# Kernel tuning notes

Measured on AMD Instinct MI355X. Metric: run time of the kernel, lower is better.

The kernel has to match this reference:

```python
import jax, jax.numpy as jnp
import numpy as np

B, L, D = 4, 2048, 512
H = 8
DH = D // H  # 64
SCALE = DH // H  # faithful to source: key.size(-1)//num_heads = 64//8 = 8 (multiplicative)
LN_EPS = 1e-5


def setup_inputs() -> dict:
    key = jax.random.key(0)
    ks = jax.random.split(key, 16)
    s = 1.0 / np.sqrt(D)
    inp = {
        "query": jax.random.normal(ks[0], (B, L, D), jnp.float32),
        "key": jax.random.normal(ks[1], (B, L, D), jnp.float32),
        "value": jax.random.normal(ks[2], (B, L, D), jnp.float32),
        "Wq": jax.random.uniform(ks[3], (D, D), jnp.float32, -s, s),
        "bq": jax.random.uniform(ks[4], (D,), jnp.float32, -s, s),
        "Wk": jax.random.uniform(ks[5], (D, D), jnp.float32, -s, s),
        "bk": jax.random.uniform(ks[6], (D,), jnp.float32, -s, s),
        "Wv": jax.random.uniform(ks[7], (D, D), jnp.float32, -s, s),
        "bv": jax.random.uniform(ks[8], (D,), jnp.float32, -s, s),
        "Wo": jax.random.uniform(ks[9], (D, D), jnp.float32, -s, s),
        "bo": jax.random.uniform(ks[10], (D,), jnp.float32, -s, s),
        "gamma": jnp.ones((D,), jnp.float32),
        "beta": jnp.zeros((D,), jnp.float32),
    }
    return inp


def _layer_norm(x, gamma, beta):
    mu = jnp.mean(x, axis=-1, keepdims=True)
    var = jnp.mean(jnp.square(x - mu), axis=-1, keepdims=True)
    return (x - mu) * jax.lax.rsqrt(var + LN_EPS) * gamma + beta


def reference(query, key, value, Wq, bq, Wk, bk, Wv, bv, Wo, bo, gamma, beta):
    res = query
    # QKV projections: [B, L, D]
    q = query @ Wq.T + bq
    k = key @ Wk.T + bk
    v = value @ Wv.T + bv
    # faithful to source: raw view(B*H, -1, DH) with NO transpose
    q = q.reshape(B * H, -1, DH)
    k = k.reshape(B * H, -1, DH)
    v = v.reshape(B * H, -1, DH)
    # bmm -> multiplicative scale -> softmax(dim=2) -> bmm
    attn = jnp.einsum('bqd,bkd->bqk', q, k) * SCALE  # [B*H, L, L]
    attn = jax.nn.softmax(attn, axis=2)
    ctx = jnp.einsum('bqk,bkd->bqd', attn, v)        # [B*H, L, DH]
    ctx = ctx.reshape(B, -1, DH * H)                  # [B, L, D]
    out = ctx @ Wo.T + bo
    out = _layer_norm(res + out, gamma, beta)
    return (out, attn)
```

## Files before the change

kernel.cpp:

```cpp
#include <hip/hip_runtime.h>

#define LSEQ 2048
#define DMODEL 512
#define DHD 64
#define SLAB (LSEQ*DHD)

typedef __attribute__((ext_vector_type(8))) short short8;
typedef __attribute__((ext_vector_type(4))) float f32x4;
typedef float f4raw __attribute__((ext_vector_type(4)));
typedef _Float16 half8 __attribute__((ext_vector_type(8)));
typedef _Float16 h4_t  __attribute__((ext_vector_type(4)));

__device__ __forceinline__ short f2bf(float x) {
    union { float f; unsigned u; } v; v.f = x;
    unsigned r = v.u + 0x7FFF + ((v.u >> 16) & 1);
    return (short)(r >> 16);
}
__device__ __forceinline__ float bf2f(short h) {
    union { float f; unsigned u; } v; v.u = ((unsigned)(unsigned short)h) << 16;
    return v.f;
}

#define GLOAD_LDS16(g, l) __builtin_amdgcn_global_load_lds( \
    (const __attribute__((address_space(1))) void*)(g),     \
    (__attribute__((address_space(3))) void*)(l), 16, 0, 0)

#define VMCNT0()  asm volatile("s_waitcnt vmcnt(0)" ::: "memory")
#define VMCNT2()  asm volatile("s_waitcnt vmcnt(2)" ::: "memory")
#define VMCNT4()  asm volatile("s_waitcnt vmcnt(4)" ::: "memory")
#define VMCNT6()  asm volatile("s_waitcnt vmcnt(6)" ::: "memory")
#define LGKM0()   asm volatile("s_waitcnt lgkmcnt(0)" ::: "memory")
#define BARRIER() do { __builtin_amdgcn_s_barrier(); __builtin_amdgcn_sched_barrier(0); } while (0)

template<int MODE>
__global__ __launch_bounds__(256) void proj_gemm(
    const float* __restrict__ A, const float* __restrict__ W,
    const float* __restrict__ bias, float* __restrict__ Cf,
    short* __restrict__ C0)
{
    __shared__ __align__(16) short Ah[64][40], Al[64][40], Bh[64][40], Bl[64][40];

    const int tid  = threadIdx.x;
    const int lane = tid & 63, wv = tid >> 6;
    const int wm = wv >> 1, wn = wv & 1;
    const int fr = lane & 15, kg = lane >> 4;
    const int m0 = blockIdx.y * 64, n0 = blockIdx.x * 64;

    f32x4 acc[2][2];
    #pragma unroll
    for (int i = 0; i < 2; ++i)
        #pragma unroll
        for (int j = 0; j < 2; ++j) { f32x4 z = {0.f,0.f,0.f,0.f}; acc[i][j] = z; }

    const int srow = tid >> 2, sc8 = (tid & 3) << 3;

    for (int kt = 0; kt < 16; ++kt) {
        __syncthreads();
        {
            const float* ap = A + (size_t)(m0 + srow) * DMODEL + kt*32 + sc8;
            float4 a0 = *(const float4*)ap;
            float4 a1 = *(const float4*)(ap + 4);
            float va[8] = {a0.x,a0.y,a0.z,a0.w,a1.x,a1.y,a1.z,a1.w};
            short8 h, l;
            #pragma unroll
            for (int j = 0; j < 8; ++j) { short hh = f2bf(va[j]); h[j] = hh; l[j] = f2bf(va[j] - bf2f(hh)); }
            *(short8*)&Ah[srow][sc8] = h; *(short8*)&Al[srow][sc8] = l;

            const float* wp = W + (size_t)(n0 + srow) * DMODEL + kt*32 + sc8;
            float4 b0 = *(const float4*)wp;
            float4 b1 = *(const float4*)(wp + 4);
            float vb[8] = {b0.x,b0.y,b0.z,b0.w,b1.x,b1.y,b1.z,b1.w};
            #pragma unroll
            for (int j = 0; j < 8; ++j) { short hh = f2bf(vb[j]); h[j] = hh; l[j] = f2bf(vb[j] - bf2f(hh)); }
            *(short8*)&Bh[srow][sc8] = h; *(short8*)&Bl[srow][sc8] = l;
        }
        __syncthreads();

        short8 ah[2], al[2], bh[2], bl[2];
        #pragma unroll
        for (int mf = 0; mf < 2; ++mf) {
            ah[mf] = *(short8*)&Ah[wm*32 + mf*16 + fr][kg*8];
            al[mf] = *(short8*)&Al[wm*32 + mf*16 + fr][kg*8];
        }
        #pragma unroll
        for (int nf = 0; nf < 2; ++nf) {
            bh[nf] = *(short8*)&Bh[wn*32 + nf*16 + fr][kg*8];
            bl[nf] = *(short8*)&Bl[wn*32 + nf*16 + fr][kg*8];
        }
        #pragma unroll
        for (int mf = 0; mf < 2; ++mf)
            #pragma unroll
            for (int nf = 0; nf < 2; ++nf) {
                acc[mf][nf] = __builtin_amdgcn_mfma_f32_16x16x32_bf16(ah[mf], bh[nf], acc[mf][nf], 0,0,0);
                acc[mf][nf] = __builtin_amdgcn_mfma_f32_16x16x32_bf16(ah[mf], bl[nf], acc[mf][nf], 0,0,0);
                acc[mf][nf] = __builtin_amdgcn_mfma_f32_16x16x32_bf16(al[mf], bh[nf], acc[mf][nf], 0,0,0);
            }
    }

    #pragma unroll
    for (int mf = 0; mf < 2; ++mf)
        #pragma unroll
        for (int nf = 0; nf < 2; ++nf) {
            const int col = n0 + wn*32 + nf*16 + fr;
            const float bv = bias[col];
            #pragma unroll
            for (int r = 0; r < 4; ++r) {
                const int row = m0 + wm*32 + mf*16 + kg*4 + r;
                const float o = acc[mf][nf][r] + bv;
                const size_t idx = (size_t)row * DMODEL + col;
                if (MODE == 0) Cf[idx] = o;
                else           ((_Float16*)C0)[idx] = (_Float16)o;
            }
        }
}

__global__ __launch_bounds__(256) void vtransf_kernel(
    const short* __restrict__ vh, short* __restrict__ vtf)
{
    __shared__ short T[64][72];
    const int tid = threadIdx.x;
    const int s  = blockIdx.y;
    const int t0 = blockIdx.x * 64;
    const size_t slab = (size_t)s * SLAB;

    {
        const int r = tid >> 2, c0 = (tid & 3) << 4;
        const short* src = vh + slab + (size_t)(t0 + r) * DHD + c0;
        short8 a = *(const short8*)src;
        short8 b = *(const short8*)(src + 8);
        *(short8*)&T[r][c0]     = a;
        *(short8*)&T[r][c0 + 8] = b;
    }
    __syncthreads();
    {
        const int kbl = tid >> 6, d = tid & 63;
        short8 o0, o1;
        #pragma unroll
        for (int j = 0; j < 8; ++j) { o0[j] = T[kbl*16 + j][d]; o1[j] = T[kbl*16 + 8 + j][d]; }
        short* dst = vtf + slab + ((size_t)((t0 >> 4) + kbl) * 64 + d) * 16;
        *(short8*)dst       = o0;
        *(short8*)(dst + 8) = o1;
    }
}

__global__ __launch_bounds__(512, 4) void attn_kernel(
    const _Float16* __restrict__ qf, const _Float16* __restrict__ kf,
    const _Float16* __restrict__ vtf,
    float* __restrict__ attn, float* __restrict__ ctx)
{
    __shared__ __align__(16) char KBuf[65536];
    __shared__ __align__(16) _Float16 PB[2][16][136];
    __shared__ float redA[8][16];
    __shared__ float mrow[16], lirow[16];

    const int tid  = threadIdx.x;
    const int lane = tid & 63, wv = tid >> 6;
    const int fr = lane & 15, kg = lane >> 4;

    const int wg  = blockIdx.x;
    const int rem = wg & 1023;
    const int q0  = (rem >> 3) << 4;
    const int bh  = ((wg >> 10) << 3) + (rem & 7);
    const size_t slab = (size_t)bh * SLAB;

    half8 qa[2];
    #pragma unroll
    for (int ks = 0; ks < 2; ++ks)
        qa[ks] = *(const half8*)(qf + slab + (size_t)(q0 + fr) * DHD + ks*32 + kg*8);

    const int srow = lane >> 3;
    const int scb  = (lane & 7) ^ srow;

    f32x4 s[16];

    #define STAGE_K(TI, CUR) { \
        _Pragma("unroll") \
        for (int j = 0; j < 2; ++j) { \
            const int b = wv*2 + j; \
            GLOAD_LDS16(kf + slab + (size_t)((TI)*128 + b*8 + srow)*DHD + scb*8, \
                        KBuf + (CUR)*16384 + b*1024); \
        } }

    STAGE_K(0, 0);
    STAGE_K(1, 1);
    STAGE_K(2, 2);

    const int klo = (wv << 4) + fr;
    const int sw  = fr & 7;
    #pragma unroll
    for (int i = 0; i < 16; ++i) {
        if (i + 3 < 16) STAGE_K(i + 3, (i + 3) & 3);

        if      (i <= 12) VMCNT6();
        else if (i == 13) VMCNT4();
        else if (i == 14) VMCNT2();
        else              VMCNT0();

        const char* rp = KBuf + (i & 3)*16384 + (klo << 7);
        half8 kb0 = *(const half8*)(rp + ((kg ^ sw) << 4));
        half8 kb1 = *(const half8*)(rp + (((4 + kg) ^ sw) << 4));

        f32x4 a = {0.f,0.f,0.f,0.f};
        a = __builtin_amdgcn_mfma_f32_16x16x32_f16(kb0, qa[0], a, 0,0,0);
        a = __builtin_amdgcn_mfma_f32_16x16x32_f16(kb1, qa[1], a, 0,0,0);
        s[i] = a;
    }
    #undef STAGE_K

    float m;
    {
        f32x4 mx = s[0];
        #pragma unroll
        for (int i = 1; i < 16; ++i) {
            mx.x = fmaxf(mx.x, s[i].x); mx.y = fmaxf(mx.y, s[i].y);
            mx.z = fmaxf(mx.z, s[i].z); mx.w = fmaxf(mx.w, s[i].w);
        }
        m = fmaxf(fmaxf(mx.x, mx.y), fmaxf(mx.z, mx.w));
        m = fmaxf(m, __shfl_xor(m, 16));
        m = fmaxf(m, __shfl_xor(m, 32));
    }
    if (lane < 16) redA[wv][lane] = m;
    __syncthreads();
    if (tid < 16) {
        float mm = redA[0][tid];
        #pragma unroll
        for (int w = 1; w < 8; ++w) mm = fmaxf(mm, redA[w][tid]);
        mrow[tid] = mm;
    }
    __syncthreads();
    m = mrow[fr];

    const float C = 8.0f * 1.44269504089f;
    float sum = 0.f;
    #pragma unroll
    for (int i = 0; i < 16; ++i) {
        f32x4 p;
        p.x = exp2f((s[i].x - m) * C);
        p.y = exp2f((s[i].y - m) * C);
        p.z = exp2f((s[i].z - m) * C);
        p.w = exp2f((s[i].w - m) * C);
        s[i] = p;
        sum += (p.x + p.y) + (p.z + p.w);
    }
    sum += __shfl_xor(sum, 16);
    sum += __shfl_xor(sum, 32);
    if (lane < 16) redA[wv][lane] = sum;
    __syncthreads();
    if (tid < 16) {
        float l = 0.f;
        #pragma unroll
        for (int w = 0; w < 8; ++w) l += redA[w][tid];
        lirow[tid] = 1.0f / l;
    }
    __syncthreads();
    const float li = lirow[fr];

    f32x4 acc[4];
    #pragma unroll
    for (int db = 0; db < 4; ++db) { f32x4 z = {0.f,0.f,0.f,0.f}; acc[db] = z; }

    const _Float16* vfb = vtf + slab;
    const int sq = tid >> 5, sc = tid & 31;
    float* abase = attn + ((size_t)bh * LSEQ + q0 + sq) * LSEQ + (sc << 2);

    int cur = 0;
    #pragma unroll
    for (int t = 0; t < 16; ++t) {
        f32x4 p = s[t];
        p.x *= li; p.y *= li; p.z *= li; p.w *= li;
        h4_t pw = { (_Float16)p.x, (_Float16)p.y, (_Float16)p.z, (_Float16)p.w };

        *(h4_t*)&PB[cur][fr][(wv << 4) + (kg << 2)] = pw;

        const _Float16* vb = vfb + ((size_t)(t*8 + wv) << 10) + (fr << 4) + (kg << 2);
        #pragma unroll
        for (int db = 0; db < 4; ++db) {
            h4_t va = *(const h4_t*)(vb + db*256);
            acc[db] = __builtin_amdgcn_mfma_f32_16x16x16f16(va, pw, acc[db], 0,0,0);
        }

        LGKM0();
        BARRIER();

        h4_t pr = *(const h4_t*)&PB[cur][sq][sc << 2];
        f4raw o = { (float)pr[0], (float)pr[1], (float)pr[2], (float)pr[3] };
        __builtin_nontemporal_store(o, (f4raw*)(abase + (size_t)t * 128));

        cur ^= 1;
    }

    __syncthreads();
    {
        float* pt = (float*)KBuf;
        #pragma unroll
        for (int db = 0; db < 4; ++db) {
            float4 o = { acc[db].x, acc[db].y, acc[db].z, acc[db].w };
            *(float4*)(pt + wv*1024 + fr*64 + db*16 + (kg << 2)) = o;
        }
    }
    __syncthreads();
    {
        float* pt = (float*)KBuf;
        const int e = tid << 1;
        const int q = e >> 6, d = e & 63;
        float2 r2 = {0.f, 0.f};
        #pragma unroll
        for (int w = 0; w < 8; ++w) {
            float2 t2 = *(float2*)(pt + w*1024 + q*64 + d);
            r2.x += t2.x; r2.y += t2.y;
        }
        *(float2*)(ctx + slab + (size_t)(q0 + q) * DHD + d) = r2;
    }
}

__global__ __launch_bounds__(128) void ln_kernel(
    const float* __restrict__ resid, const float* __restrict__ x,
    const float* __restrict__ gamma, const float* __restrict__ beta,
    float* __restrict__ out)
{
    const int row = blockIdx.x;
    const int tid = threadIdx.x;
    const size_t base = (size_t)row * DMODEL + tid*4;

    float4 v = *(const float4*)(x + base);
    float4 rq = *(const float4*)(resid + base);
    v.x += rq.x; v.y += rq.y; v.z += rq.z; v.w += rq.w;

    float s  = v.x + v.y + v.z + v.w;
    float ss = v.x*v.x + v.y*v.y + v.z*v.z + v.w*v.w;
    #pragma unroll
    for (int d = 1; d < 64; d <<= 1) { s += __shfl_xor(s, d); ss += __shfl_xor(ss, d); }

    __shared__ float red[2][2];
    const int wv = tid >> 6;
    if ((tid & 63) == 0) { red[wv][0] = s; red[wv][1] = ss; }
    __syncthreads();
    s  = red[0][0] + red[1][0];
    ss = red[0][1] + red[1][1];

    const float mu  = s * (1.0f/512.0f);
    const float var = ss * (1.0f/512.0f) - mu*mu;
    const float rs  = rsqrtf(var + 1e-5f);

    float4 g = *(const float4*)(gamma + tid*4);
    float4 b = *(const float4*)(beta + tid*4);
    float4 o;
    o.x = (v.x - mu) * rs * g.x + b.x;
    o.y = (v.y - mu) * rs * g.y + b.y;
    o.z = (v.z - mu) * rs * g.z + b.z;
    o.w = (v.w - mu) * rs * g.w + b.w;
    *(float4*)(out + base) = o;
}

extern "C" void kernel_launch(void* const* d_in, const int* in_sizes, int n_in,
                              void* d_out, int out_size, void* d_ws, size_t ws_size,
                              hipStream_t stream)
{
    const float* query = (const float*)d_in[0];
    const float* key   = (const float*)d_in[1];
    const float* value = (const float*)d_in[2];
    const float* Wq = (const float*)d_in[3];
    const float* bq = (const float*)d_in[4];
    const float* Wk = (const float*)d_in[5];
    const float* bk = (const float*)d_in[6];
    const float* Wv = (const float*)d_in[7];
    const float* bv = (const float*)d_in[8];
    const float* Wo = (const float*)d_in[9];
    const float* bo = (const float*)d_in[10];
    const float* gamma = (const float*)d_in[11];
    const float* beta  = (const float*)d_in[12];

    float* out  = (float*)d_out;
    float* attn = out + 4194304;

    const size_t NTOK = (size_t)8192 * 512;
    short* qv = (short*)d_ws;
    short* kv = qv + NTOK;
    short* vf = kv + NTOK;
    short* vtf = vf + NTOK;
    float* obuf = (float*)d_ws;

    dim3 pgrid(8, 128), pblk(256);
    proj_gemm<3><<<pgrid, pblk, 0, stream>>>(query, Wq, bq, nullptr, qv);
    proj_gemm<3><<<pgrid, pblk, 0, stream>>>(key,   Wk, bk, nullptr, kv);
    proj_gemm<3><<<pgrid, pblk, 0, stream>>>(value, Wv, bv, nullptr, vf);

    vtransf_kernel<<<dim3(32, 32), 256, 0, stream>>>(vf, vtf);

    attn_kernel<<<4096, 512, 0, stream>>>((const _Float16*)qv, (const _Float16*)kv,
                                          (const _Float16*)vtf, attn, out );

    proj_gemm<0><<<pgrid, pblk, 0, stream>>>(out , Wo, bo, obuf, nullptr);
    ln_kernel<<<8192, 128, 0, stream>>>(query, obuf, gamma, beta, out);
}
```

Measured before the change: 282.2 us.

## Process two query tiles per block, overlapping second QK^T with first PV

Each attention workgroup now handles 32 query rows as two 16-row tiles, so the grid is halved. The QK^T MFMAs and K staging for the second tile are interleaved into the PV/attn-store loop of the first tile, hiding K loads and score compute behind the V pass. This raises register pressure (two score arrays plus packed probabilities), so launch bounds drop from 4 to 2 blocks per CU. That may reduce occupancy and latency hiding.

```diff
diff --git a/kernel.cpp b/kernel.cpp
--- a/kernel.cpp
+++ b/kernel.cpp
@@ -143,7 +143,7 @@
     }
 }
 
-__global__ __launch_bounds__(512, 4) void attn_kernel(
+__global__ __launch_bounds__(512, 2) void attn_kernel(
     const _Float16* __restrict__ qf, const _Float16* __restrict__ kf,
     const _Float16* __restrict__ vtf,
     float* __restrict__ attn, float* __restrict__ ctx)
@@ -158,20 +158,23 @@
     const int fr = lane & 15, kg = lane >> 4;
 
     const int wg  = blockIdx.x;
-    const int rem = wg & 1023;
-    const int q0  = (rem >> 3) << 4;
-    const int bh  = ((wg >> 10) << 3) + (rem & 7);
+    const int rem = wg & 511;
+    const int q0  = (rem >> 3) << 5;
+    const int bh  = ((wg >> 9) << 3) + (rem & 7);
     const size_t slab = (size_t)bh * SLAB;
 
-    half8 qa[2];
-    #pragma unroll
-    for (int ks = 0; ks < 2; ++ks)
-        qa[ks] = *(const half8*)(qf + slab + (size_t)(q0 + fr) * DHD + ks*32 + kg*8);
+    half8 qaA[2], qaB[2];
+    #pragma unroll
+    for (int ks = 0; ks < 2; ++ks) {
+        qaA[ks] = *(const half8*)(qf + slab + (size_t)(q0 + fr) * DHD + ks*32 + kg*8);
+        qaB[ks] = *(const half8*)(qf + slab + (size_t)(q0 + 16 + fr) * DHD + ks*32 + kg*8);
+    }
 
     const int srow = lane >> 3;
     const int scb  = (lane & 7) ^ srow;
-
-    f32x4 s[16];
+    const int klo = (wv << 4) + fr;
+    const int sw  = fr & 7;
+    const float C = 8.0f * 1.44269504089f;
 
     #define STAGE_K(TI, CUR) { \
         _Pragma("unroll") \
@@ -180,112 +183,118 @@
             GLOAD_LDS16(kf + slab + (size_t)((TI)*128 + b*8 + srow)*DHD + scb*8, \
                         KBuf + (CUR)*16384 + b*1024); \
         } }
-
-    STAGE_K(0, 0);
-    STAGE_K(1, 1);
-    STAGE_K(2, 2);
-
-    const int klo = (wv << 4) + fr;
-    const int sw  = fr & 7;
+    #define KFRAGS(IDX, K0, K1) { \
+        const char* rp_ = KBuf + ((IDX) & 3)*16384 + (klo << 7); \
+        K0 = *(const half8*)(rp_ + ((kg ^ sw) << 4)); \
+        K1 = *(const half8*)(rp_ + (((4 + kg) ^ sw) << 4)); }
+
+    f32x4 sA[16];
+    STAGE_K(0, 0); STAGE_K(1, 1); STAGE_K(2, 2);
     #pragma unroll
     for (int i = 0; i < 16; ++i) {
         if (i + 3 < 16) STAGE_K(i + 3, (i + 3) & 3);
-
         if      (i <= 12) VMCNT6();
         else if (i == 13) VMCNT4();
         else if (i == 14) VMCNT2();
         else              VMCNT0();
-
-        const char* rp = KBuf + (i & 3)*16384 + (klo << 7);
-        half8 kb0 = *(const half8*)(rp + ((kg ^ sw) << 4));
-        half8 kb1 = *(const half8*)(rp + (((4 + kg) ^ sw) << 4));
-
+        half8 kb0, kb1; KFRAGS(i, kb0, kb1);
         f32x4 a = {0.f,0.f,0.f,0.f};
-        a = __builtin_amdgcn_mfma_f32_16x16x32_f16(kb0, qa[0], a, 0,0,0);
-        a = __builtin_amdgcn_mfma_f32_16x16x32_f16(kb1, qa[1], a, 0,0,0);
-        s[i] = a;
-    }
-    #undef STAGE_K
-
-    float m;
-    {
-        f32x4 mx = s[0];
+        a = __builtin_amdgcn_mfma_f32_16x16x32_f16(kb0, qaA[0], a, 0,0,0);
+        a = __builtin_amdgcn_mfma_f32_16x16x32_f16(kb1, qaA[1], a, 0,0,0);
+        sA[i] = a;
+    }
+
+    h4_t paA[16];
+    {
+        f32x4 mx = sA[0];
         #pragma unroll
         for (int i = 1; i < 16; ++i) {
-            mx.x = fmaxf(mx.x, s[i].x); mx.y = fmaxf(mx.y, s[i].y);
-            mx.z = fmaxf(mx.z, s[i].z); mx.w = fmaxf(mx.w, s[i].w);
-        }
-        m = fmaxf(fmaxf(mx.x, mx.y), fmaxf(mx.z, mx.w));
+            mx.x = fmaxf(mx.x, sA[i].x); mx.y = fmaxf(mx.y, sA[i].y);
+            mx.z = fmaxf(mx.z, sA[i].z); mx.w = fmaxf(mx.w, sA[i].w);
+        }
+        float m = fmaxf(fmaxf(mx.x, mx.y), fmaxf(mx.z, mx.w));
         m = fmaxf(m, __shfl_xor(m, 16));
         m = fmaxf(m, __shfl_xor(m, 32));
-    }
-    if (lane < 16) redA[wv][lane] = m;
-    __syncthreads();
-    if (tid < 16) {
-        float mm = redA[0][tid];
-        #pragma unroll
-        for (int w = 1; w < 8; ++w) mm = fmaxf(mm, redA[w][tid]);
-        mrow[tid] = mm;
-    }
-    __syncthreads();
-    m = mrow[fr];
-
-    const float C = 8.0f * 1.44269504089f;
-    float sum = 0.f;
-    #pragma unroll
-    for (int i = 0; i < 16; ++i) {
-        f32x4 p;
-        p.x = exp2f((s[i].x - m) * C);
-        p.y = exp2f((s[i].y - m) * C);
-        p.z = exp2f((s[i].z - m) * C);
-        p.w = exp2f((s[i].w - m) * C);
-        s[i] = p;
-        sum += (p.x + p.y) + (p.z + p.w);
-    }
-    sum += __shfl_xor(sum, 16);
-    sum += __shfl_xor(sum, 32);
-    if (lane < 16) redA[wv][lane] = sum;
-    __syncthreads();
-    if (tid < 16) {
-        float l = 0.f;
-        #pragma unroll
-        for (int w = 0; w < 8; ++w) l += redA[w][tid];
-        lirow[tid] = 1.0f / l;
-    }
-    __syncthreads();
-    const float li = lirow[fr];
+        if (lane < 16) redA[wv][lane] = m;
+        __syncthreads();
+        if (tid < 16) {
+            float mm = redA[0][tid];
+            #pragma unroll
+            for (int w = 1; w < 8; ++w) mm = fmaxf(mm, redA[w][tid]);
+            mrow[tid] = mm;
+        }
+        __syncthreads();
+        m = mrow[fr];
+
+        float sum = 0.f;
+        #pragma unroll
+        for (int i = 0; i < 16; ++i) {
+            f32x4 p;
+            p.x = exp2f((sA[i].x - m) * C);
+            p.y = exp2f((sA[i].y - m) * C);
+            p.z = exp2f((sA[i].z - m) * C);
+            p.w = exp2f((sA[i].w - m) * C);
+            sA[i] = p;
+            sum += (p.x + p.y) + (p.z + p.w);
+        }
+        sum += __shfl_xor(sum, 16);
+        sum += __shfl_xor(sum, 32);
+        if (lane < 16) redA[wv][lane] = sum;
+        __syncthreads();
+        if (tid < 16) {
+            float l = 0.f;
+            #pragma unroll
+            for (int w = 0; w < 8; ++w) l += redA[w][tid];
+            lirow[tid] = 1.0f / l;
+        }
+        __syncthreads();
+        const float li = lirow[fr];
+        #pragma unroll
+        for (int i = 0; i < 16; ++i) {
+            paA[i][0] = (_Float16)(sA[i].x * li);
+            paA[i][1] = (_Float16)(sA[i].y * li);
+            paA[i][2] = (_Float16)(sA[i].z * li);
+            paA[i][3] = (_Float16)(sA[i].w * li);
+        }
+    }
 
     f32x4 acc[4];
     #pragma unroll
     for (int db = 0; db < 4; ++db) { f32x4 z = {0.f,0.f,0.f,0.f}; acc[db] = z; }
-
     const _Float16* vfb = vtf + slab;
     const int sq = tid >> 5, sc = tid & 31;
-    float* abase = attn + ((size_t)bh * LSEQ + q0 + sq) * LSEQ + (sc << 2);
-
+    float* abaseA = attn + ((size_t)bh * LSEQ + q0 + sq) * LSEQ + (sc << 2);
+    float* abaseB = abaseA + (size_t)16 * LSEQ;
+
+    f32x4 sB[16];
     int cur = 0;
+    STAGE_K(0, 0); STAGE_K(1, 1); STAGE_K(2, 2);
     #pragma unroll
     for (int t = 0; t < 16; ++t) {
-        f32x4 p = s[t];
-        p.x *= li; p.y *= li; p.z *= li; p.w *= li;
-        h4_t pw = { (_Float16)p.x, (_Float16)p.y, (_Float16)p.z, (_Float16)p.w };
-
+        if (t + 3 < 16) STAGE_K(t + 3, (t + 3) & 3);
+        if      (t <= 12) VMCNT6();
+        else if (t == 13) VMCNT4();
+        else if (t == 14) VMCNT2();
+        else              VMCNT0();
+        half8 kb0, kb1; KFRAGS(t, kb0, kb1);
+        f32x4 a = {0.f,0.f,0.f,0.f};
+        a = __builtin_amdgcn_mfma_f32_16x16x32_f16(kb0, qaB[0], a, 0,0,0);
+        a = __builtin_amdgcn_mfma_f32_16x16x32_f16(kb1, qaB[1], a, 0,0,0);
+        sB[t] = a;
+
+        h4_t pw = paA[t];
         *(h4_t*)&PB[cur][fr][(wv << 4) + (kg << 2)] = pw;
-
         const _Float16* vb = vfb + ((size_t)(t*8 + wv) << 10) + (fr << 4) + (kg << 2);
         #pragma unroll
         for (int db = 0; db < 4; ++db) {
             h4_t va = *(const h4_t*)(vb + db*256);
             acc[db] = __builtin_amdgcn_mfma_f32_16x16x16f16(va, pw, acc[db], 0,0,0);
         }
-
         LGKM0();
         BARRIER();
-
         h4_t pr = *(const h4_t*)&PB[cur][sq][sc << 2];
         f4raw o = { (float)pr[0], (float)pr[1], (float)pr[2], (float)pr[3] };
-        __builtin_nontemporal_store(o, (f4raw*)(abase + (size_t)t * 128));
-
+        __builtin_nontemporal_store(o, (f4raw*)(abaseA + (size_t)t * 128));
         cur ^= 1;
     }
 
@@ -311,6 +320,106 @@
         }
         *(float2*)(ctx + slab + (size_t)(q0 + q) * DHD + d) = r2;
     }
+    __syncthreads();
+
+    h4_t paB[16];
+    {
+        f32x4 mx = sB[0];
+        #pragma unroll
+        for (int i = 1; i < 16; ++i) {
+            mx.x = fmaxf(mx.x, sB[i].x); mx.y = fmaxf(mx.y, sB[i].y);
+            mx.z = fmaxf(mx.z, sB[i].z); mx.w = fmaxf(mx.w, sB[i].w);
+        }
+        float m = fmaxf(fmaxf(mx.x, mx.y), fmaxf(mx.z, mx.w));
+        m = fmaxf(m, __shfl_xor(m, 16));
+        m = fmaxf(m, __shfl_xor(m, 32));
+        if (lane < 16) redA[wv][lane] = m;
+        __syncthreads();
+        if (tid < 16) {
+            float mm = redA[0][tid];
+            #pragma unroll
+            for (int w = 1; w < 8; ++w) mm = fmaxf(mm, redA[w][tid]);
+            mrow[tid] = mm;
+        }
+        __syncthreads();
+        m = mrow[fr];
+
+        float sum = 0.f;
+        #pragma unroll
+        for (int i = 0; i < 16; ++i) {
+            f32x4 p;
+            p.x = exp2f((sB[i].x - m) * C);
+            p.y = exp2f((sB[i].y - m) * C);
+            p.z = exp2f((sB[i].z - m) * C);
+            p.w = exp2f((sB[i].w - m) * C);
+            sB[i] = p;
+            sum += (p.x + p.y) + (p.z + p.w);
+        }
+        sum += __shfl_xor(sum, 16);
+        sum += __shfl_xor(sum, 32);
+        if (lane < 16) redA[wv][lane] = sum;
+        __syncthreads();
+        if (tid < 16) {
+            float l = 0.f;
+            #pragma unroll
+            for (int w = 0; w < 8; ++w) l += redA[w][tid];
+            lirow[tid] = 1.0f / l;
+        }
+        __syncthreads();
+        const float li = lirow[fr];
+        #pragma unroll
+        for (int i = 0; i < 16; ++i) {
+            paB[i][0] = (_Float16)(sB[i].x * li);
+            paB[i][1] = (_Float16)(sB[i].y * li);
+            paB[i][2] = (_Float16)(sB[i].z * li);
+            paB[i][3] = (_Float16)(sB[i].w * li);
+        }
+    }
+
+    #pragma unroll
+    for (int db = 0; db < 4; ++db) { f32x4 z = {0.f,0.f,0.f,0.f}; acc[db] = z; }
+    #pragma unroll
+    for (int t = 0; t < 16; ++t) {
+        h4_t pw = paB[t];
+        *(h4_t*)&PB[cur][fr][(wv << 4) + (kg << 2)] = pw;
+        const _Float16* vb = vfb + ((size_t)(t*8 + wv) << 10) + (fr << 4) + (kg << 2);
+        #pragma unroll
+        for (int db = 0; db < 4; ++db) {
+            h4_t va = *(const h4_t*)(vb + db*256);
+            acc[db] = __builtin_amdgcn_mfma_f32_16x16x16f16(va, pw, acc[db], 0,0,0);
+        }
+        LGKM0();
+        BARRIER();
+        h4_t pr = *(const h4_t*)&PB[cur][sq][sc << 2];
+        f4raw o = { (float)pr[0], (float)pr[1], (float)pr[2], (float)pr[3] };
+        __builtin_nontemporal_store(o, (f4raw*)(abaseB + (size_t)t * 128));
+        cur ^= 1;
+    }
+
+    __syncthreads();
+    {
+        float* pt = (float*)KBuf;
+        #pragma unroll
+        for (int db = 0; db < 4; ++db) {
+            float4 o = { acc[db].x, acc[db].y, acc[db].z, acc[db].w };
+            *(float4*)(pt + wv*1024 + fr*64 + db*16 + (kg << 2)) = o;
+        }
+    }
+    __syncthreads();
+    {
+        float* pt = (float*)KBuf;
+        const int e = tid << 1;
+        const int q = e >> 6, d = e & 63;
+        float2 r2 = {0.f, 0.f};
+        #pragma unroll
+        for (int w = 0; w < 8; ++w) {
+            float2 t2 = *(float2*)(pt + w*1024 + q*64 + d);
+            r2.x += t2.x; r2.y += t2.y;
+        }
+        *(float2*)(ctx + slab + (size_t)(q0 + 16 + q) * DHD + d) = r2;
+    }
+    #undef STAGE_K
+    #undef KFRAGS
 }
 
 __global__ __launch_bounds__(128) void ln_kernel(
@@ -387,7 +496,7 @@
 
     vtransf_kernel<<<dim3(32, 32), 256, 0, stream>>>(vf, vtf);
 
-    attn_kernel<<<4096, 512, 0, stream>>>((const _Float16*)qv, (const _Float16*)kv,
+    attn_kernel<<<2048, 512, 0, stream>>>((const _Float16*)qv, (const _Float16*)kv,
                                           (const _Float16*)vtf, attn, out );
 
     proj_gemm<0><<<pgrid, pblk, 0, stream>>>(out , Wo, bo, obuf, nullptr);
```

Measured after the change: 339.7 us. +20.3%, slower.
